# Kernel tuning notes

Hardware: AMD Instinct MI355X
Metric: run time of the kernel (lower is better)

The kernel has to match this reference:

```python
import jax, jax.numpy as jnp
import numpy as np

B, N, D = 2, 2048, 1024
H = 16
HD = D // H  # 64
N_CTX = 256


def setup_inputs() -> dict:
    key = jax.random.key(0)
    ks = jax.random.split(key, 10)
    x = jax.random.normal(ks[0], (B, N, D), dtype=jnp.float32)
    ctx_ppr = jax.random.uniform(ks[1], (N_CTX,), dtype=jnp.float32, minval=1e-4, maxval=1.0)
    ctx_trust = jax.random.uniform(ks[2], (N_CTX,), dtype=jnp.float32)
    attn_mask = jax.random.randint(ks[3], (N, N), 0, 2).astype(jnp.bool_)
    # parameters (nn.Linear convention: y = x @ W.T + b)
    s_in = 1.0 / np.sqrt(D)
    W_in = jax.random.uniform(ks[4], (3 * D, D), dtype=jnp.float32, minval=-s_in, maxval=s_in)
    b_in = jax.random.uniform(ks[5], (3 * D,), dtype=jnp.float32, minval=-s_in, maxval=s_in)
    W_out = jax.random.uniform(ks[6], (D, D), dtype=jnp.float32, minval=-s_in, maxval=s_in)
    b_out = jax.random.uniform(ks[7], (D,), dtype=jnp.float32, minval=-s_in, maxval=s_in)
    log_ppr_alpha = jnp.ones((1,), jnp.float32) * 0.1
    trust_scale = jnp.ones((1,), jnp.float32) * 0.1
    return {"x": x, "ctx_ppr": ctx_ppr, "ctx_trust": ctx_trust, "n_ctx": N_CTX,
            "attn_mask": attn_mask, "W_in": W_in, "b_in": b_in,
            "W_out": W_out, "b_out": b_out,
            "log_ppr_alpha": log_ppr_alpha, "trust_scale": trust_scale}


def reference(x, ctx_ppr, ctx_trust, n_ctx, attn_mask, W_in, b_in, W_out, b_out,
              log_ppr_alpha, trust_scale):
    Bx, Nx, Dx = x.shape
    scale = HD ** -0.5
    qkv = x @ W_in.T + b_in  # [B,N,3D]
    q, k, v = jnp.split(qkv, 3, axis=-1)
    q = q.reshape(Bx, Nx, H, HD).transpose(0, 2, 1, 3)  # [B,H,N,d]
    k = k.reshape(Bx, Nx, H, HD).transpose(0, 2, 1, 3)
    v = v.reshape(Bx, Nx, H, HD).transpose(0, 2, 1, 3)
    if n_ctx > 0:
        gate = jax.nn.sigmoid(trust_scale[0] * ctx_trust)  # [n_ctx]
        gate_full = jnp.concatenate([gate, jnp.ones(Nx - n_ctx, x.dtype)])
        v = v * gate_full[None, None, :, None]
    logits = jnp.einsum('bhqd,bhkd->bhqk', q, k) * scale
    if n_ctx > 0:
        bias = log_ppr_alpha[0] * jnp.log(jnp.clip(ctx_ppr, 1e-8, None))
        col_bias = jnp.concatenate([bias, jnp.zeros(Nx - n_ctx, x.dtype)])
        logits = logits + col_bias[None, None, None, :]
    logits = jnp.where(attn_mask[None, None, :, :], -jnp.inf, logits)
    weights = jax.nn.softmax(logits, axis=-1)
    out = jnp.einsum('bhqk,bhkd->bhqd', weights, v)
    out = out.transpose(0, 2, 1, 3).reshape(Bx, Nx, Dx)
    return out @ W_out.T + b_out
```

## Files before the change

kernel.cpp:

```cpp
#include <hip/hip_runtime.h>
#include <hip/hip_bf16.h>
#include <math.h>

#define B_   2
#define N_   2048
#define D_   1024
#define H_   16
#define TD_  3072
#define LOG2E 1.44269504088896340736f
#define SCALE_Q (0.125f * LOG2E)

typedef short  bf16x8 __attribute__((ext_vector_type(8)));
typedef _Float16 f16x8 __attribute__((ext_vector_type(8)));
typedef _Float16 f16x4 __attribute__((ext_vector_type(4)));
typedef float  f32x4  __attribute__((ext_vector_type(4)));
typedef float  f32x16 __attribute__((ext_vector_type(16)));

#define MFMA32B(a, b, c)  __builtin_amdgcn_mfma_f32_32x32x16_bf16(a, b, c, 0, 0, 0)
#define MFMA32H(a, b, c)  __builtin_amdgcn_mfma_f32_32x32x16_f16(a, b, c, 0, 0, 0)

__device__ __forceinline__ ushort f2bf(float f) {
    union { float f; unsigned u; } v; v.f = f;
    unsigned r = (v.u + 0x7fffu + ((v.u >> 16) & 1u)) >> 16;
    return (ushort)r;
}
__device__ __forceinline__ unsigned pkrtz(float a, float b) {
    typedef __fp16 h2 __attribute__((ext_vector_type(2)));
    union { h2 h; unsigned u; } c;
    c.h = __builtin_amdgcn_cvt_pkrtz(a, b);
    return c.u;
}
__device__ __forceinline__ void async16(const void* g, void* l) {
    __builtin_amdgcn_global_load_lds(
        (const __attribute__((address_space(1))) unsigned*)g,
        (__attribute__((address_space(3))) unsigned*)l, 16, 0, 0);
}
__device__ __forceinline__ void plswap(unsigned &a, unsigned &b) {
    auto r = __builtin_amdgcn_permlane32_swap((int)a, (int)b, false, false);
    a = (unsigned)r[0]; b = (unsigned)r[1];
}

__global__ __launch_bounds__(256) void preprocess(
    const float* __restrict__ x, const float* __restrict__ W_in,
    const float* __restrict__ W_out, const float* __restrict__ ctx_ppr,
    const float* __restrict__ log_alpha, const int* __restrict__ n_ctx_p,
    const int* __restrict__ mask,
    ushort* __restrict__ xb, ushort* __restrict__ wib, ushort* __restrict__ wob,
    float* __restrict__ biasrow, unsigned* __restrict__ maskbits)
{
    const int J0 = 1048576, J1 = 786432, J2 = 262144, JM = 131072, JB = 2048;
    int t = blockIdx.x * 256 + threadIdx.x;
    if (t < J0 + J1 + J2) {
        const float* src; ushort* dst; int i = t;
        if (i < J0)           { src = x;      dst = xb;  }
        else if (i < J0 + J1) { i -= J0;      src = W_in;  dst = wib; }
        else                  { i -= J0 + J1; src = W_out; dst = wob; }
        float4 v = ((const float4*)src)[i];
        ushort4 o;
        o.x = f2bf(v.x); o.y = f2bf(v.y); o.z = f2bf(v.z); o.w = f2bf(v.w);
        ((ushort4*)dst)[i] = o;
    } else if (t < J0 + J1 + J2 + JM) {
        int i = t - (J0 + J1 + J2);
        const int4* m = (const int4*)(mask + (size_t)i * 32);
        unsigned bits = 0u;
        #pragma unroll
        for (int j = 0; j < 8; ++j) {
            int4 w = m[j];
            bits |= (w.x != 0 ? 1u : 0u) << (j * 4 + 0);
            bits |= (w.y != 0 ? 1u : 0u) << (j * 4 + 1);
            bits |= (w.z != 0 ? 1u : 0u) << (j * 4 + 2);
            bits |= (w.w != 0 ? 1u : 0u) << (j * 4 + 3);
        }
        maskbits[i] = bits;
    } else if (t < J0 + J1 + J2 + JM + JB) {
        int k = t - (J0 + J1 + J2 + JM);
        int nc = n_ctx_p[0];
        float bv = 0.f;
        if (k < nc) bv = log_alpha[0] * __log2f(fmaxf(ctx_ppr[k], 1e-8f));
        biasrow[k] = bv;
    }
}

template<int BCOL, int MODE>
__global__ __launch_bounds__(256) void gemm32(
    const ushort* __restrict__ A, const ushort* __restrict__ Bw,
    const float* __restrict__ bias, float* __restrict__ Cout,
    ushort* __restrict__ qkout, _Float16* __restrict__ vTout,
    int Ncol, int K,
    const float* __restrict__ ctx_trust, const float* __restrict__ trust_scale,
    const int* __restrict__ n_ctx_p)
{
    constexpr int CT = BCOL / 64;
    constexpr int LB = BCOL / 32;
    __shared__ ushort tA[2][128 * 64];
    __shared__ ushort tB[2][BCOL * 64];
    const int tid = threadIdx.x;
    const int lane = tid & 63, wv = tid >> 6;
    const int q31 = lane & 31, hi = lane >> 5;
    const int rh = wv >> 1, ch = wv & 1;
    const int id = blockIdx.x;
    const int wg = (id & 7) * 64 + (id >> 3);
    const int row0 = (wg >> 4) * 128, col0 = (wg & 15) * BCOL;

    const int swz = q31 & 7;
    int offAr[2], offBr[CT];
    #pragma unroll
    for (int rt = 0; rt < 2; ++rt) offAr[rt] = (rh * 64 + rt * 32 + q31) * 64;
    #pragma unroll
    for (int ct = 0; ct < CT; ++ct) offBr[ct] = (ch * (BCOL / 2) + ct * 32 + q31) * 64;

    f32x16 acc[2][CT];
    #pragma unroll
    for (int i = 0; i < 2; ++i)
        #pragma unroll
        for (int j = 0; j < CT; ++j) acc[i][j] = (f32x16)(0.f);

    int arow[4], asg[4], brow[LB], bsg[LB];
    #pragma unroll
    for (int r2 = 0; r2 < 4; ++r2) {
        int g = r2 * 256 + tid;
        arow[r2] = g >> 3; asg[r2] = ((g & 7) ^ ((g >> 3) & 7)) << 3;
    }
    #pragma unroll
    for (int r2 = 0; r2 < LB; ++r2) {
        int g = r2 * 256 + tid;
        brow[r2] = g >> 3; bsg[r2] = ((g & 7) ^ ((g >> 3) & 7)) << 3;
    }
    const ushort* Ab = A + (size_t)row0 * K;
    const ushort* Bb = Bw + (size_t)col0 * K;

    auto issue = [&](int ktile, int bufi) {
        const int kt = ktile * 64;
        #pragma unroll
        for (int r2 = 0; r2 < 4; ++r2)
            async16(Ab + (size_t)arow[r2] * K + kt + asg[r2],
                    &tA[bufi][(r2 * 256 + tid) * 8]);
        #pragma unroll
        for (int r2 = 0; r2 < LB; ++r2)
            async16(Bb + (size_t)brow[r2] * K + kt + bsg[r2],
                    &tB[bufi][(r2 * 256 + tid) * 8]);
    };

    issue(0, 0);
    const int NIT = K / 64;
    #pragma unroll 1
    for (int it = 0; it < NIT; ++it) {
        const int cur = it & 1;
        asm volatile("s_barrier" ::: "memory");
        if (it + 1 < NIT) {
            issue(it + 1, cur ^ 1);
            if constexpr (BCOL == 192)
                asm volatile("s_waitcnt vmcnt(10)" ::: "memory");
            else
                asm volatile("s_waitcnt vmcnt(6)" ::: "memory");
        } else {
            asm volatile("s_waitcnt vmcnt(0)" ::: "memory");
        }
        asm volatile("s_barrier" ::: "memory");

        const ushort* KA = tA[cur];
        const ushort* KB = tB[cur];
        __builtin_amdgcn_s_setprio(1);
        #pragma unroll
        for (int kk = 0; kk < 4; ++kk) {
            const int gr = ((kk * 2 + hi) ^ swz) << 3;
            bf16x8 af[2], bfv[CT];
            #pragma unroll
            for (int rt = 0; rt < 2; ++rt)
                af[rt] = *(const bf16x8*)&KA[offAr[rt] + gr];
            #pragma unroll
            for (int ct = 0; ct < CT; ++ct)
                bfv[ct] = *(const bf16x8*)&KB[offBr[ct] + gr];
            #pragma unroll
            for (int rt = 0; rt < 2; ++rt)
                #pragma unroll
                for (int ct = 0; ct < CT; ++ct)
                    acc[rt][ct] = MFMA32B(af[rt], bfv[ct], acc[rt][ct]);
        }
        __builtin_amdgcn_s_setprio(0);
    }

    const int nctx = n_ctx_p ? n_ctx_p[0] : 0;
    const float ts = trust_scale ? trust_scale[0] : 0.f;
    #pragma unroll
    for (int ct = 0; ct < CT; ++ct) {
        const int col = col0 + ch * (BCOL / 2) + ct * 32 + q31;
        const float bv = bias[col];
        #pragma unroll
        for (int rt = 0; rt < 2; ++rt) {
            const int rb0 = row0 + rh * 64 + rt * 32 + 4 * hi;
            f32x16 a = acc[rt][ct];
            if (MODE == 0) {
                #pragma unroll
                for (int g2 = 0; g2 < 4; ++g2)
                    #pragma unroll
                    for (int r = 0; r < 4; ++r)
                        Cout[(size_t)(rb0 + 8 * g2 + r) * Ncol + col] = a[g2 * 4 + r] + bv;
            } else if (col < D_) {
                #pragma unroll
                for (int g2 = 0; g2 < 4; ++g2)
                    #pragma unroll
                    for (int r = 0; r < 4; ++r)
                        qkout[(size_t)(rb0 + 8 * g2 + r) * 2048 + col] =
                            f2bf((a[g2 * 4 + r] + bv) * SCALE_Q);
            } else if (col < 2 * D_) {
                #pragma unroll
                for (int g2 = 0; g2 < 4; ++g2)
                    #pragma unroll
                    for (int r = 0; r < 4; ++r)
                        qkout[(size_t)(rb0 + 8 * g2 + r) * 2048 + col] =
                            f2bf(a[g2 * 4 + r] + bv);
            } else {
                const int vc = col - 2 * D_;
                const int hh = vc >> 6, dim = vc & 63;
                const int bb = row0 >> 11;
                #pragma unroll
                for (int g2 = 0; g2 < 4; ++g2) {
                    const int nbase = (rb0 + 8 * g2) & (N_ - 1);
                    ushort4 o;
                    #pragma unroll
                    for (int r = 0; r < 4; ++r) {
                        float v = a[g2 * 4 + r] + bv;
                        const int n = nbase + r;
                        if (n < nctx)
                            v *= 1.f / (1.f + __expf(-ts * ctx_trust[n]));
                        _Float16 hv = (_Float16)v;
                        ((ushort*)&o)[r] = *(ushort*)&hv;
                    }
                    *(ushort4*)&vTout[((size_t)(bb * 16 + hh) * 64 + dim) * 2048 + nbase] = o;
                }
            }
        }
    }
}

__global__ __launch_bounds__(256, 4) void attn(
    const ushort* __restrict__ qkb,
    const _Float16* __restrict__ vT,
    const unsigned* __restrict__ maskbits,
    const float* __restrict__ biasrow,
    const int* __restrict__ n_ctx_p,
    _Float16* __restrict__ op0,
    _Float16* __restrict__ op1,
    float* __restrict__ lpart)
{
    __shared__ ushort   Kt[3][64 * 64];
    __shared__ _Float16 Vt[2][64 * 64];
    const int tid = threadIdx.x;
    const int lane = tid & 63, wv = tid >> 6;
    const int q31 = lane & 31, hi = lane >> 5;
    const int b = blockIdx.y >> 4, h = blockIdx.y & 15;
    const int q0w = blockIdx.x * 128 + wv * 32;
    const int kh = blockIdx.z;
    const int kbase = kh << 10;
    const int nctx = n_ctx_p[0];

    const int lin = blockIdx.x + (blockIdx.y << 4) + (blockIdx.z << 9);
    const int rot = ((lin >> 8) << 2) & 15;

    union fi { float f; int i; };
    fi ng; ng.f = -1e30f;
    const int NEGI = ng.i;

    bf16x8 qf[4];
    {
        const ushort* qrow = qkb + (size_t)(b * N_ + q0w + q31) * 2048 + h * 64;
        #pragma unroll
        for (int ks = 0; ks < 4; ++ks)
            qf[ks] = *(const bf16x8*)(qrow + ks * 16 + hi * 8);
    }
    const size_t kgbase = (size_t)(b * N_ + kbase) * 2048 + 1024 + h * 64;
    const _Float16* vbase = vT + (size_t)((b * 16 + h) * 64) * 2048 + kbase;
    const unsigned* mrow = maskbits + (size_t)(q0w + q31) * 64 + (kbase >> 5);

    int goff[2], ldso[2];
    #pragma unroll
    for (int r2 = 0; r2 < 2; ++r2) {
        int g = r2 * 256 + tid, row = g >> 3, sg = (g & 7) ^ (row & 7);
        goff[r2] = row * 2048 + sg * 8;
        ldso[r2] = g * 8;
    }

    f32x16 O[2];
    O[0] = (f32x16)(0.f); O[1] = (f32x16)(0.f);
    float lrun = 0.f;

    const int cp0 = rot, cp1 = (rot + 1) & 15;
    uint2 mcur = *(const uint2*)&mrow[cp0 * 2];
    asm volatile("" ::: "memory");
    {
        const ushort* gp0 = qkb + kgbase + (size_t)cp0 * (64 * 2048);
        #pragma unroll
        for (int r2 = 0; r2 < 2; ++r2) async16(gp0 + goff[r2], &Kt[0][ldso[r2]]);
        const _Float16* vp = vbase + cp0 * 64;
        #pragma unroll
        for (int r2 = 0; r2 < 2; ++r2) async16(vp + goff[r2], &Vt[0][ldso[r2]]);
        const ushort* gp1 = qkb + kgbase + (size_t)cp1 * (64 * 2048);
        #pragma unroll
        for (int r2 = 0; r2 < 2; ++r2) async16(gp1 + goff[r2], &Kt[1][ldso[r2]]);
    }

    const int swz = q31 & 7;
    int kb = 0;
    #pragma unroll 1
    for (int ci = 0; ci < 16; ++ci) {
        asm volatile("s_barrier" ::: "memory");
        uint2 mnext = mcur;
        if (ci < 15) {
            const int cpv = (ci + 1 + rot) & 15;
            mnext = *(const uint2*)&mrow[cpv * 2];
            asm volatile("" ::: "memory");
            const _Float16* vp = vbase + cpv * 64;
            #pragma unroll
            for (int r2 = 0; r2 < 2; ++r2)
                async16(vp + goff[r2], &Vt[(ci + 1) & 1][ldso[r2]]);
        }
        if (ci < 14) {
            int nb = kb + 2; if (nb >= 3) nb -= 3;
            const int cpk = (ci + 2 + rot) & 15;
            const ushort* gp = qkb + kgbase + (size_t)cpk * (64 * 2048);
            #pragma unroll
            for (int r2 = 0; r2 < 2; ++r2)
                async16(gp + goff[r2], &Kt[nb][ldso[r2]]);
        }
        if (ci < 14)       asm volatile("s_waitcnt vmcnt(7)" ::: "memory");
        else if (ci == 14) asm volatile("s_waitcnt vmcnt(5)" ::: "memory");
        else               asm volatile("s_waitcnt vmcnt(0)" ::: "memory");
        asm volatile("s_barrier" ::: "memory");

        const ushort*   KT = Kt[kb];
        const _Float16* VT = Vt[ci & 1];
        const int cp = (ci + rot) & 15;
        const int c0g = kbase + cp * 64;
        const bool has_bias = (c0g < nctx);
        float lsum = 0.f;

        #pragma unroll
        for (int t = 0; t < 2; ++t) {
            f32x16 S = (f32x16)(0.f);
            const int rbase = (t * 32 + q31) * 64;
            __builtin_amdgcn_s_setprio(1);
            #pragma unroll
            for (int ks = 0; ks < 4; ++ks) {
                bf16x8 kf = *(const bf16x8*)&KT[rbase + (((ks * 2 + hi) ^ swz) << 3)];
                S = MFMA32B(kf, qf[ks], S);
            }
            __builtin_amdgcn_s_setprio(0);

            const unsigned msh = (t ? mcur.y : mcur.x) >> (hi * 4);
            unsigned pk[8];
            float lt = 0.f;
            #pragma unroll
            for (int g = 0; g < 4; ++g) {
                f32x4 bb;
                if (has_bias)
                    bb = *(const f32x4*)&biasrow[c0g + t * 32 + g * 8 + hi * 4];
                float pr[4];
                #pragma unroll
                for (int r = 0; r < 4; ++r) {
                    const int br = r + 8 * g;
                    float s = S[g * 4 + r];
                    if (has_bias) s += bb[r];
                    int mi = ((int)(msh << (31 - br))) >> 31;
                    fi su; su.f = s;
                    su.i = (mi & NEGI) | (su.i & ~mi);
                    pr[r] = __builtin_amdgcn_exp2f(su.f);
                }
                lt += (pr[0] + pr[1]) + (pr[2] + pr[3]);
                pk[g * 2 + 0] = pkrtz(pr[0], pr[1]);
                pk[g * 2 + 1] = pkrtz(pr[2], pr[3]);
            }
            lsum += lt;

            __builtin_amdgcn_s_setprio(1);
            #pragma unroll
            for (int kss = 0; kss < 2; ++kss) {
                const int ks = 2 * t + kss, lo4 = kss * 4;
                unsigned w0 = pk[lo4 + 0], w1 = pk[lo4 + 1];
                unsigned w2 = pk[lo4 + 2], w3 = pk[lo4 + 3];
                plswap(w0, w2);
                plswap(w1, w3);
                union { f16x8 v; unsigned u[4]; } frag;
                frag.u[0] = w0; frag.u[1] = w1;
                frag.u[2] = w2; frag.u[3] = w3;
                #pragma unroll
                for (int t2 = 0; t2 < 2; ++t2) {
                    const int vb = (t2 * 32 + q31) * 64;
                    union { f16x8 v; int4 i4; } vf;
                    vf.i4 = *(const int4*)&VT[vb + (((ks * 2 + hi) ^ swz) << 3)];
                    O[t2] = MFMA32H(vf.v, frag.v, O[t2]);
                }
            }
            __builtin_amdgcn_s_setprio(0);
        }
        lrun += lsum;
        mcur = mnext;
        kb = kb + 1; if (kb >= 3) kb -= 3;
    }

    float l = lrun + __shfl_xor(lrun, 32);
    float inv = 1.f / l;
    _Float16* orow = (kh ? op1 : op0)
                   + (size_t)(b * N_ + q0w + q31) * 1024 + h * 64;
    #pragma unroll
    for (int t = 0; t < 2; ++t)
        #pragma unroll
        for (int g = 0; g < 4; ++g) {
            ushort4 o;
            #pragma unroll
            for (int r = 0; r < 4; ++r) {
                _Float16 hv = (_Float16)(O[t][g * 4 + r] * inv);
                ((ushort*)&o)[r] = *(ushort*)&hv;
            }
            *(ushort4*)&orow[t * 32 + g * 8 + hi * 4] = o;
        }
    if (hi == 0)
        lpart[(kh << 16) + (b * 16 + h) * 2048 + q0w + q31] = l;
}

__global__ __launch_bounds__(256) void combine(
    const _Float16* __restrict__ op0, const _Float16* __restrict__ op1,
    const float* __restrict__ lpart, ushort* __restrict__ attb)
{
    int t = blockIdx.x * 256 + threadIdx.x;
    size_t idx = (size_t)t * 4;
    int col = (int)(idx & 1023);
    int row = (int)(idx >> 10);
    int h = col >> 6;
    int b = row >> 11, q = row & 2047;
    int lidx = (b * 16 + h) * 2048 + q;
    float l0 = lpart[lidx], l1 = lpart[65536 + lidx];
    float inv = 1.f / (l0 + l1);
    float w0 = l0 * inv, w1 = l1 * inv;
    f16x4 a0 = *(const f16x4*)(op0 + idx);
    f16x4 a1 = *(const f16x4*)(op1 + idx);
    ushort4 o;
    #pragma unroll
    for (int r = 0; r < 4; ++r)
        ((ushort*)&o)[r] = f2bf((float)a0[r] * w0 + (float)a1[r] * w1);
    *(ushort4*)(attb + idx) = o;
}

extern "C" void kernel_launch(void* const* d_in, const int* in_sizes, int n_in,
                              void* d_out, int out_size, void* d_ws, size_t ws_size,
                              hipStream_t stream)
{
    const float* x         = (const float*)d_in[0];
    const float* ctx_ppr   = (const float*)d_in[1];
    const float* ctx_trust = (const float*)d_in[2];
    const int*   n_ctx_p   = (const int*)d_in[3];
    const int*   attn_mask = (const int*)d_in[4];
    const float* W_in      = (const float*)d_in[5];
    const float* b_in      = (const float*)d_in[6];
    const float* W_out     = (const float*)d_in[7];
    const float* b_out     = (const float*)d_in[8];
    const float* log_alpha = (const float*)d_in[9];
    const float* trust_sc  = (const float*)d_in[10];
    float* out = (float*)d_out;

    char* ws = (char*)d_ws;
    ushort*    xb       = (ushort*)ws;    ws += (size_t)4096 * 1024 * 2;
    ushort*    wib      = (ushort*)ws;    ws += (size_t)3072 * 1024 * 2;
    ushort*    wob      = (ushort*)ws;    ws += (size_t)1024 * 1024 * 2;
    ushort*    qkb      = (ushort*)ws;    ws += (size_t)4096 * 2048 * 2;
    _Float16*  vT       = (_Float16*)ws;  ws += (size_t)2048 * 2048 * 2;
    ushort*    attbuf   = (ushort*)ws;    ws += (size_t)4096 * 1024 * 2;
    float*     biasrow  = (float*)ws;     ws += 2048 * 4;
    unsigned*  maskbits = (unsigned*)ws;  ws += (size_t)2048 * 64 * 4;

    _Float16* op0   = (_Float16*)xb;
    _Float16* op1   = (_Float16*)attbuf;
    float*    lpart = (float*)wib;

    hipLaunchKernelGGL(preprocess, dim3(8712), dim3(256), 0, stream,
                       x, W_in, W_out, ctx_ppr, log_alpha, n_ctx_p, attn_mask,
                       xb, wib, wob, biasrow, maskbits);

    hipLaunchKernelGGL((gemm32<192, 1>), dim3(512), dim3(256), 0, stream,
                       xb, wib, b_in, (float*)nullptr, qkb, vT, TD_, 1024,
                       ctx_trust, trust_sc, n_ctx_p);

    hipLaunchKernelGGL(attn, dim3(16, 32, 2), dim3(256), 0, stream,
                       qkb, vT, maskbits, biasrow, n_ctx_p, op0, op1, lpart);

    hipLaunchKernelGGL(combine, dim3(4096), dim3(256), 0, stream,
                       op0, op1, lpart, attbuf);

    hipLaunchKernelGGL((gemm32<64, 0>), dim3(512), dim3(256), 0, stream,
                       attbuf, wob, b_out, out, (ushort*)nullptr, (_Float16*)nullptr,
                       1024, 1024, ctx_trust, trust_sc, n_ctx_p);
}
```

Measured before the change: 248.2 us.

## Fuse split-K attention combine into output projection GEMM

Replaces the separate combine kernel and output-projection GEMM with one kernel. It merges the two partial attention outputs using the lpart weights while building the bf16 A fragments, then multiplies by W_out via MFMA. This removes an intermediate bf16 buffer round-trip and one launch. In exchange, A operands are read straight from global memory without LDS reuse, with a simpler 64x64 tiling than the previous GEMM.

```diff
diff --git a/kernel.cpp b/kernel.cpp
--- a/kernel.cpp
+++ b/kernel.cpp
@@ -418,27 +418,92 @@
         lpart[(kh << 16) + (b * 16 + h) * 2048 + q0w + q31] = l;
 }
 
-__global__ __launch_bounds__(256) void combine(
+__global__ __launch_bounds__(256) void outproj(
     const _Float16* __restrict__ op0, const _Float16* __restrict__ op1,
-    const float* __restrict__ lpart, ushort* __restrict__ attb)
+    const float* __restrict__ lpart, const ushort* __restrict__ wob,
+    const float* __restrict__ bias, float* __restrict__ out)
 {
-    int t = blockIdx.x * 256 + threadIdx.x;
-    size_t idx = (size_t)t * 4;
-    int col = (int)(idx & 1023);
-    int row = (int)(idx >> 10);
-    int h = col >> 6;
-    int b = row >> 11, q = row & 2047;
-    int lidx = (b * 16 + h) * 2048 + q;
-    float l0 = lpart[lidx], l1 = lpart[65536 + lidx];
-    float inv = 1.f / (l0 + l1);
-    float w0 = l0 * inv, w1 = l1 * inv;
-    f16x4 a0 = *(const f16x4*)(op0 + idx);
-    f16x4 a1 = *(const f16x4*)(op1 + idx);
-    ushort4 o;
-    #pragma unroll
-    for (int r = 0; r < 4; ++r)
-        ((ushort*)&o)[r] = f2bf((float)a0[r] * w0 + (float)a1[r] * w1);
-    *(ushort4*)(attb + idx) = o;
+    __shared__ ushort tB[2][64 * 32];
+    const int tid = threadIdx.x;
+    const int lane = tid & 63, wv = tid >> 6;
+    const int q31 = lane & 31, hi = lane >> 5;
+    const int rh = wv >> 1, ch = wv & 1;
+    const int id = blockIdx.x;
+    const int wg = (id & 7) * 128 + (id >> 3);
+    const int rp = wg >> 4, cp = wg & 15;
+
+    const int rg = rp * 64 + rh * 32 + q31;
+    const int bq = rg >> 11, qq = rg & 2047;
+    const int col = cp * 64 + ch * 32 + q31;
+    const float bv = bias[col];
+
+    const ushort* bsrc = wob + (size_t)(cp * 64 + (tid >> 2)) * 1024
+                       + (((tid & 3) ^ ((tid >> 2) & 3)) << 3);
+    const _Float16* a0p = op0 + (size_t)rg * 1024 + hi * 8;
+    const _Float16* a1p = op1 + (size_t)rg * 1024 + hi * 8;
+    const float* lp0 = lpart + (size_t)bq * 16 * 2048 + qq;
+    const float* lp1 = lp0 + 65536;
+
+    f32x16 acc = (f32x16)(0.f);
+    const int swzB = q31 & 3;
+    const int browB = (ch * 32 + q31) * 32;
+
+    async16(bsrc, &tB[0][tid * 8]);
+    f16x8 o0c[2], o1c[2];
+    #pragma unroll
+    for (int kk = 0; kk < 2; ++kk) {
+        o0c[kk] = *(const f16x8*)(a0p + kk * 16);
+        o1c[kk] = *(const f16x8*)(a1p + kk * 16);
+    }
+    float l0c = lp0[0], l1c = lp1[0];
+
+    #pragma unroll 1
+    for (int t = 0; t < 32; ++t) {
+        asm volatile("s_barrier" ::: "memory");
+        f16x8 o0n[2] = { o0c[0], o0c[1] }, o1n[2] = { o1c[0], o1c[1] };
+        float l0n = l0c, l1n = l1c;
+        if (t + 1 < 32) {
+            const int ktn = (t + 1) * 32;
+            async16(bsrc + ktn, &tB[(t + 1) & 1][tid * 8]);
+            #pragma unroll
+            for (int kk = 0; kk < 2; ++kk) {
+                o0n[kk] = *(const f16x8*)(a0p + ktn + kk * 16);
+                o1n[kk] = *(const f16x8*)(a1p + ktn + kk * 16);
+            }
+            const int hn = (t + 1) >> 1;
+            l0n = lp0[hn * 2048];
+            l1n = lp1[hn * 2048];
+            asm volatile("s_waitcnt vmcnt(7)" ::: "memory");
+        } else {
+            asm volatile("s_waitcnt vmcnt(0)" ::: "memory");
+        }
+        asm volatile("s_barrier" ::: "memory");
+
+        const float inv = 1.f / (l0c + l1c);
+        const float w0 = l0c * inv, w1 = l1c * inv;
+        const ushort* KB = tB[t & 1];
+        #pragma unroll
+        for (int kk = 0; kk < 2; ++kk) {
+            union { bf16x8 v; ushort u[8]; } af;
+            #pragma unroll
+            for (int j = 0; j < 8; ++j) {
+                float a = (float)o0c[kk][j] * w0 + (float)o1c[kk][j] * w1;
+                af.u[j] = f2bf(a);
+            }
+            bf16x8 bf = *(const bf16x8*)&KB[browB + (((kk * 2 + hi) ^ swzB) << 3)];
+            acc = MFMA32B(af.v, bf, acc);
+        }
+        o0c[0] = o0n[0]; o0c[1] = o0n[1];
+        o1c[0] = o1n[0]; o1c[1] = o1n[1];
+        l0c = l0n; l1c = l1n;
+    }
+
+    const int rb0 = rp * 64 + rh * 32 + 4 * hi;
+    #pragma unroll
+    for (int g2 = 0; g2 < 4; ++g2)
+        #pragma unroll
+        for (int r = 0; r < 4; ++r)
+            out[(size_t)(rb0 + 8 * g2 + r) * 1024 + col] = acc[g2 * 4 + r] + bv;
 }
 
 extern "C" void kernel_launch(void* const* d_in, const int* in_sizes, int n_in,
@@ -483,10 +548,6 @@
     hipLaunchKernelGGL(attn, dim3(16, 32, 2), dim3(256), 0, stream,
                        qkb, vT, maskbits, biasrow, n_ctx_p, op0, op1, lpart);
 
-    hipLaunchKernelGGL(combine, dim3(4096), dim3(256), 0, stream,
-                       op0, op1, lpart, attbuf);
-
-    hipLaunchKernelGGL((gemm32<64, 0>), dim3(512), dim3(256), 0, stream,
-                       attbuf, wob, b_out, out, (ushort*)nullptr, (_Float16*)nullptr,
-                       1024, 1024, ctx_trust, trust_sc, n_ctx_p);
-}
+    hipLaunchKernelGGL(outproj, dim3(1024), dim3(256), 0, stream,
+                       op0, op1, lpart, wob, b_out, out);
+}
```

After: 294.7 us. 18.8% more time.
